# Kernel tuning notes

Hardware: AMD Instinct MI355X
Metric: run time of the kernel (lower is better)

Reference implementation:

```python
import jax, jax.numpy as jnp
import numpy as np

# ---- model hyperparams (from init_kwargs) ----
N_USERS = 200000
N_ITEMS = 100000
DIM = 64
NNZ = 3000000
BATCH = 4096
N_HOPS = 3          # context_hops
EPS = 0.1           # SimGCL perturbation magnitude
TEMP = 0.2          # tau
CL_RATE = 0.5       # lamb
DECAY = 1e-4        # l2


def setup_inputs() -> dict:
    key = jax.random.key(0)
    k = jax.random.split(key, 8)
    user_embed = (jax.random.normal(k[0], (N_USERS, DIM), dtype=jnp.float32) * 0.01)
    item_embed = (jax.random.normal(k[1], (N_ITEMS, DIM), dtype=jnp.float32) * 0.01)
    N = N_USERS + N_ITEMS
    # COO normalized adjacency (buffer, not a parameter in the torch module)
    adj_rows = jax.random.randint(k[2], (NNZ,), 0, N)
    adj_cols = jax.random.randint(k[3], (NNZ,), 0, N)
    adj_vals = jax.random.uniform(k[4], (NNZ,), dtype=jnp.float32) * 0.2
    # unique index batches (torch code calls torch.unique for the CL loss;
    # sampling without replacement makes skipping unique exact, since the
    # InfoNCE mean is permutation invariant)
    users = jax.random.permutation(k[5], N_USERS)[:BATCH].astype(jnp.int32)
    pos_items = jax.random.permutation(k[6], N_ITEMS)[:BATCH].astype(jnp.int32)
    neg_items = jax.random.randint(k[7], (BATCH,), 0, N_ITEMS)
    return {"user_embed": user_embed, "item_embed": item_embed,
            "adj_vals": adj_vals, "adj_rows": adj_rows, "adj_cols": adj_cols,
            "users": users, "pos_items": pos_items, "neg_items": neg_items}


def _spmm(vals, rows, cols, x):
    # torch.sparse.mm(A, x) with A in COO form: out[r] += v * x[c]
    return jax.ops.segment_sum(vals[:, None] * x[cols], rows, num_segments=x.shape[0])


def _gcn(user_embed, item_embed, vals, rows, cols, perturbed, key):
    ego = jnp.concatenate([user_embed, item_embed], axis=0)  # [N, D]
    acc = jnp.zeros_like(ego)
    for h in range(N_HOPS):
        ego = _spmm(vals, rows, cols, ego)
        if perturbed:
            noise = jax.random.uniform(jax.random.fold_in(key, h), ego.shape, dtype=ego.dtype)
            noise = noise / jnp.maximum(jnp.linalg.norm(noise, axis=-1, keepdims=True), 1e-12)
            ego = ego + jnp.sign(ego) * noise * EPS
        acc = acc + ego
    mean = acc / N_HOPS   # stack + mean over hops == running-sum / n_hops
    return mean[:N_USERS], mean[N_USERS:]


def _info_nce(v1, v2, temp):
    v1 = v1 / jnp.maximum(jnp.linalg.norm(v1, axis=1, keepdims=True), 1e-12)
    v2 = v2 / jnp.maximum(jnp.linalg.norm(v2, axis=1, keepdims=True), 1e-12)
    pos = jnp.exp(jnp.sum(v1 * v2, axis=-1) / temp)              # [B]
    ttl = jnp.sum(jnp.exp((v1 @ v2.T) / temp), axis=1)           # [B]
    return jnp.mean(-jnp.log(pos / ttl + 1e-5))


def reference(user_embed, item_embed, adj_vals, adj_rows, adj_cols, users, pos_items, neg_items):
    # --- recommendation branch (no perturbation) ---
    ru, ri = _gcn(user_embed, item_embed, adj_vals, adj_rows, adj_cols, False, jax.random.key(0))
    ue, pe, ne = ru[users], ri[pos_items], ri[neg_items]
    pos_score = jnp.sum(ue * pe, axis=1)
    neg_score = jnp.sum(ue * ne, axis=1)
    rec_loss = jnp.mean(-jnp.log(1e-5 + jax.nn.sigmoid(pos_score - neg_score)))
    reg_loss = DECAY * (jnp.linalg.norm(ue) + jnp.linalg.norm(pe))  # Frobenius norms
    # --- contrastive branch: two perturbed views of the whole GCN ---
    u1, i1 = _gcn(user_embed, item_embed, adj_vals, adj_rows, adj_cols, True, jax.random.key(101))
    u2, i2 = _gcn(user_embed, item_embed, adj_vals, adj_rows, adj_cols, True, jax.random.key(202))
    cl_loss = CL_RATE * (_info_nce(u1[users], u2[users], TEMP)
                         + _info_nce(i1[pos_items], i2[pos_items], TEMP))
    return rec_loss + reg_loss + cl_loss
```

## Files before the change

### kernel.cpp

```cpp
#include <hip/hip_runtime.h>
#include <stdint.h>

#define NUSERS  200000
#define NITEMS  100000
#define NTOT    300000
#define DIM     64
#define NU64    (NUSERS * DIM)
#define NNZC    3000000
#define BATCH   4096
#define B64     (BATCH * DIM)
#define EPSP    0.1f
#define INV_TEMP 5.0f
#define SCAN_ELEMS 1024
#define GELEMS ((size_t)7 * B64 + 2 * BATCH + 8)
#define BCAP   163840

#define BSHIFT 11
#define BROWS  (1 << BSHIFT)
#define NB     ((NTOT + BROWS - 1) / BROWS)
#define CHUNK  4096
#define NCHUNK ((NNZC + CHUNK - 1) / CHUNK)
#define NH     (NB * NCHUNK)
#define CASTB  ((NTOT * DIM) / 2048)
#define Z4V    (NTOT / 4)
#define Z4T    ((2 * BATCH + 8) / 4)
#define ZVB    ((Z4V + 511) / 512)
#define ZTB    ((Z4T + 511) / 512)

typedef short bf16x8 __attribute__((ext_vector_type(8)));
typedef float f32x4  __attribute__((ext_vector_type(4)));

__device__ __forceinline__ float b2f(unsigned short h) {
  return __uint_as_float(((uint32_t)h) << 16);
}
__device__ __forceinline__ unsigned short f2b(float f) {
  uint32_t b = __float_as_uint(f);
  uint32_t r = b + 0x7FFFu + ((b >> 16) & 1u);
  return (unsigned short)(r >> 16);
}

__device__ __forceinline__ uint32_t mix32(uint32_t h) {
  h ^= h >> 16; h *= 0x85EBCA6Bu;
  h ^= h >> 13; h *= 0xC2B2AE35u;
  h ^= h >> 16;
  return h;
}
__device__ __forceinline__ uint32_t noise_key(uint32_t seed, uint32_t hop) {
  return mix32(seed * 0x9E3779B9u + hop * 0x85EBCA6Bu + 0x1BD11BDAu);
}
__device__ __forceinline__ float fast_unif(uint32_t key, uint32_t e) {
  uint32_t h = mix32(key + e * 0x9E3779B9u);
  return __uint_as_float((h >> 9) | 0x3F800000u) - 1.0f;
}
__device__ __forceinline__ float n_ss4(uint32_t key, uint32_t rq, float4& u) {
  uint32_t h = mix32(key + rq * 0x9E3779B9u);
  u.x = ((float)(h & 255u)         + 0.5f) * (1.0f / 256.0f);
  u.y = ((float)((h >> 8) & 255u)  + 0.5f) * (1.0f / 256.0f);
  u.z = ((float)((h >> 16) & 255u) + 0.5f) * (1.0f / 256.0f);
  u.w = ((float)(h >> 24)          + 0.5f) * (1.0f / 256.0f);
  return u.x * u.x + u.y * u.y + u.z * u.z + u.w * u.w;
}

__device__ __forceinline__ float sgnf(float a) {
  return (a > 0.f) ? 1.f : ((a < 0.f) ? -1.f : 0.f);
}

__global__ __launch_bounds__(256) void partA_cast(
    const int* __restrict__ rows, int* __restrict__ Hcnt,
    const float* __restrict__ uemb, const float* __restrict__ iemb,
    unsigned short* __restrict__ X0,
    int* __restrict__ vflag, float* __restrict__ ttlz) {
  int blk = blockIdx.x;
  if (blk >= NCHUNK + CASTB + ZVB) {
    int i4 = (blk - NCHUNK - CASTB - ZVB) * 512 + threadIdx.x;
    float4 z = make_float4(0.f, 0.f, 0.f, 0.f);
    if (i4 < Z4T) ((float4*)ttlz)[i4] = z;
    i4 += 256;
    if (i4 < Z4T) ((float4*)ttlz)[i4] = z;
    return;
  }
  if (blk >= NCHUNK + CASTB) {
    int i4 = (blk - NCHUNK - CASTB) * 512 + threadIdx.x;
    int4 z = make_int4(0, 0, 0, 0);
    if (i4 < Z4V) ((int4*)vflag)[i4] = z;
    i4 += 256;
    if (i4 < Z4V) ((int4*)vflag)[i4] = z;
    return;
  }
  if (blk >= NCHUNK) {
    int base = (blk - NCHUNK) * 2048 + threadIdx.x * 8;
    const float* src = (base < NU64) ? (uemb + base) : (iemb + (base - NU64));
    float4 f0 = ((const float4*)src)[0];
    float4 f1 = ((const float4*)src)[1];
    uint4 o;
    o.x = ((uint32_t)f2b(f0.y) << 16) | f2b(f0.x);
    o.y = ((uint32_t)f2b(f0.w) << 16) | f2b(f0.z);
    o.z = ((uint32_t)f2b(f1.y) << 16) | f2b(f1.x);
    o.w = ((uint32_t)f2b(f1.w) << 16) | f2b(f1.z);
    *(uint4*)(X0 + base) = o;
    return;
  }
  __shared__ int bc[256];
  int c = blk, t = threadIdx.x;
  bc[t] = 0;
  __syncthreads();
  int base = c * CHUNK;
  for (int i = t; i < CHUNK; i += 256) {
    int e = base + i;
    if (e < NNZC) atomicAdd(&bc[rows[e] >> BSHIFT], 1);
  }
  __syncthreads();
  if (t < NB) Hcnt[t * NCHUNK + c] = bc[t];
}

__global__ void scan_block(const int* __restrict__ cnt, int* __restrict__ out,
                           int* __restrict__ bsums, int n) {
  __shared__ int tmp[SCAN_ELEMS];
  int base = blockIdx.x * SCAN_ELEMS;
  int t = threadIdx.x;
  #pragma unroll
  for (int q = 0; q < 4; ++q) {
    int k = t + q * 256, i = base + k;
    tmp[k] = (i < n) ? cnt[i] : 0;
  }
  __syncthreads();
  for (int off = 1; off < SCAN_ELEMS; off <<= 1) {
    int v[4];
    #pragma unroll
    for (int q = 0; q < 4; ++q) {
      int k = t + q * 256;
      v[q] = (k >= off) ? tmp[k - off] : 0;
    }
    __syncthreads();
    #pragma unroll
    for (int q = 0; q < 4; ++q) tmp[t + q * 256] += v[q];
    __syncthreads();
  }
  #pragma unroll
  for (int q = 0; q < 4; ++q) {
    int k = t + q * 256, i = base + k;
    if (i < n) out[i] = (k == 0) ? 0 : tmp[k - 1];
  }
  if (t == 0) bsums[blockIdx.x] = tmp[SCAN_ELEMS - 1];
}

__global__ void add_offsets_scan(int* __restrict__ out,
                                 const int* __restrict__ bsums,
                                 int n, int nb) {
  __shared__ int tmp[512];
  int t = threadIdx.x;
  tmp[t] = (t < nb) ? bsums[t] : 0;
  tmp[t + 256] = (t + 256 < nb) ? bsums[t + 256] : 0;
  __syncthreads();
  for (int off = 1; off < 512; off <<= 1) {
    int v0 = (t >= off) ? tmp[t - off] : 0;
    int v1 = (t + 256 >= off) ? tmp[t + 256 - off] : 0;
    __syncthreads();
    tmp[t] += v0; tmp[t + 256] += v1;
    __syncthreads();
  }
  int i = blockIdx.x * 256 + t;
  if (i < n) {
    int b = i >> 10;
    out[i] += (b == 0) ? 0 : tmp[b - 1];
  }
}

__global__ void add_offsets_emit_scan(int* __restrict__ vmap,
                                      const int* __restrict__ bsums,
                                      const int* __restrict__ vflag,
                                      int* __restrict__ vlist,
                                      int* __restrict__ nV, int nb) {
  __shared__ int tmp[512];
  int t = threadIdx.x;
  tmp[t] = (t < nb) ? bsums[t] : 0;
  tmp[t + 256] = (t + 256 < nb) ? bsums[t + 256] : 0;
  __syncthreads();
  for (int off = 1; off < 512; off <<= 1) {
    int v0 = (t >= off) ? tmp[t - off] : 0;
    int v1 = (t + 256 >= off) ? tmp[t + 256 - off] : 0;
    __syncthreads();
    tmp[t] += v0; tmp[t + 256] += v1;
    __syncthreads();
  }
  int i = blockIdx.x * 256 + t;
  if (i >= NTOT) return;
  int b = i >> 10;
  int m = vmap[i] + ((b == 0) ? 0 : tmp[b - 1]);
  vmap[i] = m;
  if (vflag[i] && m < BCAP) vlist[m] = i;
  if (i == NTOT - 1) {
    int tot = m + vflag[i];
    nV[0] = (tot > BCAP) ? BCAP : tot;
  }
}

__global__ __launch_bounds__(256) void partB(const float* __restrict__ vals,
                                             const int* __restrict__ rows,
                                             const int* __restrict__ cols,
                                             const int* __restrict__ Hofs,
                                             int2* __restrict__ midp,
                                             int* __restrict__ midr) {
  __shared__ int2 stv[CHUNK];
  __shared__ int  str_[CHUNK];
  __shared__ int  cnt[256];
  __shared__ int  sc[256];
  __shared__ int  adj[NB];
  int c = blockIdx.x, t = threadIdx.x;
  cnt[t] = 0;
  __syncthreads();
  int base = c * CHUNK;
  for (int i = t; i < CHUNK; i += 256) {
    int e = base + i;
    if (e < NNZC) atomicAdd(&cnt[rows[e] >> BSHIFT], 1);
  }
  __syncthreads();
  sc[t] = cnt[t];
  __syncthreads();
  for (int off = 1; off < 256; off <<= 1) {
    int u = (t >= off) ? sc[t - off] : 0;
    __syncthreads();
    sc[t] += u;
    __syncthreads();
  }
  int excl = sc[t] - cnt[t];
  cnt[t] = excl;
  if (t < NB) adj[t] = Hofs[t * NCHUNK + c] - excl;
  __syncthreads();
  for (int i = t; i < CHUNK; i += 256) {
    int e = base + i;
    if (e < NNZC) {
      int r = rows[e];
      int b = r >> BSHIFT;
      int p = atomicAdd(&cnt[b], 1);
      stv[p] = make_int2(__float_as_int(vals[e]), cols[e] * DIM);
      str_[p] = r;
    }
  }
  __syncthreads();
  int n = NNZC - base;
  if (n > CHUNK) n = CHUNK;
  for (int p = t; p < n; p += 256) {
    int r = str_[p];
    int b = r >> BSHIFT;
    int dst = adj[b] + p;
    midp[dst] = stv[p];
    midr[dst] = r;
  }
}

__global__ __launch_bounds__(256) void partC(const int2* __restrict__ midp,
                                             const int* __restrict__ midr,
                                             const int* __restrict__ Hofs,
                                             int* __restrict__ rs,
                                             int2* __restrict__ pairs) {
  __shared__ int h[BROWS];
  __shared__ int tsum[256];
  int b = blockIdx.x, t = threadIdx.x;
  int row0 = b << BSHIFT;
  for (int i = t; i < BROWS; i += 256) h[i] = 0;
  __syncthreads();
  int s = Hofs[b * NCHUNK];
  int e = (b + 1 < NB) ? Hofs[(b + 1) * NCHUNK] : NNZC;
  for (int p = s + t; p < e; p += 256)
    atomicAdd(&h[midr[p] - row0], 1);
  __syncthreads();
  int loc[8], run = 0;
  #pragma unroll
  for (int k = 0; k < 8; ++k) { loc[k] = run; run += h[t * 8 + k]; }
  tsum[t] = run;
  __syncthreads();
  for (int off = 1; off < 256; off <<= 1) {
    int v = (t >= off) ? tsum[t - off] : 0;
    __syncthreads();
    tsum[t] += v;
    __syncthreads();
  }
  int baseT = (t == 0) ? 0 : tsum[t - 1];
  #pragma unroll
  for (int k = 0; k < 8; ++k) {
    int i = t * 8 + k;
    int pos = s + baseT + loc[k];
    if (row0 + i < NTOT) rs[row0 + i] = pos;
    h[i] = pos;
  }
  if (b == NB - 1 && t == 0) rs[NTOT] = NNZC;
  __syncthreads();
  for (int p = s + t; p < e; p += 256) {
    int r = midr[p];
    int2 v = midp[p];
    int pos = atomicAdd(&h[r - row0], 1);
    pairs[pos] = v;
  }
}

__global__ __launch_bounds__(256) void mark_v(const int* __restrict__ u,
                                              const int* __restrict__ p,
                                              const int* __restrict__ n,
                                              const int* __restrict__ rs,
                                              const int2* __restrict__ pairs,
                                              int* __restrict__ vflag) {
  int i = blockIdx.x * 256 + threadIdx.x;
  if (i >= 3 * BATCH) return;
  int v = (i < BATCH) ? u[i]
        : (i < 2 * BATCH) ? (NUSERS + p[i - BATCH])
        : (NUSERS + n[i - 2 * BATCH]);
  vflag[v] = 1;
  int s = rs[v], e = rs[v + 1];
  for (int j = s; j < e; ++j) vflag[(unsigned)pairs[j].y >> 6] = 1;
}

__global__ __launch_bounds__(256) void spmm_hop3(
    const int2* __restrict__ pairs, const int* __restrict__ rs,
    const unsigned short* __restrict__ x,
    unsigned short* __restrict__ A, unsigned short* __restrict__ A1,
    unsigned short* __restrict__ A2) {
  const uint32_t k101 = noise_key(101u, 0u);
  const uint32_t k202 = noise_key(202u, 0u);
  int tid  = threadIdx.x;
  int lane = tid & 63;
  int q    = lane & 15;
  int wave = (blockIdx.x * 256 + tid) >> 6;
  int r    = wave * 4 + (lane >> 4);
  int s    = rs[r];
  int e    = rs[r + 1];
  int q4 = q * 4;
  float a0[4] = {0.f, 0.f, 0.f, 0.f};
  for (int j = s; j < e; j += 8) {
    int2 p[8];
    #pragma unroll
    for (int k = 0; k < 8; ++k)
      p[k] = (j + k < e) ? pairs[j + k] : make_int2(0, 0);
    #pragma unroll
    for (int k = 0; k < 8; ++k) {
      float v = __int_as_float(p[k].x);
      unsigned o = (unsigned)(p[k].y + q4);
      ushort4 h = *(const ushort4*)(x + o);
      a0[0] = fmaf(v, b2f(h.x), a0[0]); a0[1] = fmaf(v, b2f(h.y), a0[1]);
      a0[2] = fmaf(v, b2f(h.z), a0[2]); a0[3] = fmaf(v, b2f(h.w), a0[3]);
    }
  }
  int ebase = r * 64 + q4;
  ushort4 st;
  st.x = f2b(a0[0]); st.y = f2b(a0[1]); st.z = f2b(a0[2]); st.w = f2b(a0[3]);
  *(ushort4*)(A + ebase) = st;
  float a[4] = {b2f(st.x), b2f(st.y), b2f(st.z), b2f(st.w)};
  float4 u1, u2;
  float s1 = n_ss4(k101, (uint32_t)(r * 16 + q), u1);
  float s2 = n_ss4(k202, (uint32_t)(r * 16 + q), u2);
  #pragma unroll
  for (int m = 1; m < 16; m <<= 1) {
    s1 += __shfl_xor(s1, m);
    s2 += __shfl_xor(s2, m);
  }
  float sc1 = EPSP / fmaxf(sqrtf(s1), 1e-12f);
  float sc2 = EPSP / fmaxf(sqrtf(s2), 1e-12f);
  float g0 = sgnf(a[0]), g1 = sgnf(a[1]), g2 = sgnf(a[2]), g3 = sgnf(a[3]);
  ushort4 o1, o2;
  o1.x = f2b(fmaf(g0 * u1.x, sc1, a[0]));
  o1.y = f2b(fmaf(g1 * u1.y, sc1, a[1]));
  o1.z = f2b(fmaf(g2 * u1.z, sc1, a[2]));
  o1.w = f2b(fmaf(g3 * u1.w, sc1, a[3]));
  o2.x = f2b(fmaf(g0 * u2.x, sc2, a[0]));
  o2.y = f2b(fmaf(g1 * u2.y, sc2, a[1]));
  o2.z = f2b(fmaf(g2 * u2.z, sc2, a[2]));
  o2.w = f2b(fmaf(g3 * u2.w, sc2, a[3]));
  *(ushort4*)(A1 + ebase) = o1;
  *(ushort4*)(A2 + ebase) = o2;
}

__global__ __launch_bounds__(256) void spmm_sub3t(
    const int2* __restrict__ pairs, const int* __restrict__ rs,
    const int* __restrict__ vlist, const int* __restrict__ nVp,
    const unsigned short* __restrict__ A,
    const unsigned short* __restrict__ A1,
    const unsigned short* __restrict__ A2,
    unsigned short* __restrict__ y0, unsigned short* __restrict__ y1,
    unsigned short* __restrict__ y2) {
  int nV = nVp[0];
  if (blockIdx.x * 16 >= nV) return;
  int tid  = threadIdx.x;
  int lane = tid & 63;
  int q    = lane & 15;
  int wave = (blockIdx.x * 256 + tid) >> 6;
  int slot = wave * 4 + (lane >> 4);
  if (slot >= nV) return;
  int v = vlist[slot];
  int s = rs[v];
  int e = rs[v + 1];
  int q4 = q * 4;
  float c0[4] = {0,0,0,0}, c1[4] = {0,0,0,0}, c2[4] = {0,0,0,0};
  for (int j = s; j < e; j += 8) {
    int2 p[8];
    #pragma unroll
    for (int k = 0; k < 8; ++k)
      p[k] = (j + k < e) ? pairs[j + k] : make_int2(0, 0);
    #pragma unroll
    for (int k = 0; k < 8; ++k) {
      float vv = __int_as_float(p[k].x);
      unsigned o = (unsigned)(p[k].y + q4);
      ushort4 h0 = *(const ushort4*)(A  + o);
      ushort4 h1 = *(const ushort4*)(A1 + o);
      ushort4 h2 = *(const ushort4*)(A2 + o);
      c0[0] = fmaf(vv, b2f(h0.x), c0[0]); c0[1] = fmaf(vv, b2f(h0.y), c0[1]);
      c0[2] = fmaf(vv, b2f(h0.z), c0[2]); c0[3] = fmaf(vv, b2f(h0.w), c0[3]);
      c1[0] = fmaf(vv, b2f(h1.x), c1[0]); c1[1] = fmaf(vv, b2f(h1.y), c1[1]);
      c1[2] = fmaf(vv, b2f(h1.z), c1[2]); c1[3] = fmaf(vv, b2f(h1.w), c1[3]);
      c2[0] = fmaf(vv, b2f(h2.x), c2[0]); c2[1] = fmaf(vv, b2f(h2.y), c2[1]);
      c2[2] = fmaf(vv, b2f(h2.z), c2[2]); c2[3] = fmaf(vv, b2f(h2.w), c2[3]);
    }
  }
  int ob = slot * 64 + q4;
  int en = v * 64 + q4;
  {
    ushort4 st;
    st.x = f2b(c0[0]); st.y = f2b(c0[1]); st.z = f2b(c0[2]); st.w = f2b(c0[3]);
    *(ushort4*)(y0 + ob) = st;
  }
  {
    uint32_t key = noise_key(101u, 1u);
    float u[4], ss = 0.f;
    #pragma unroll
    for (int k = 0; k < 4; ++k) {
      u[k] = fast_unif(key, (uint32_t)(en + k));
      ss += u[k] * u[k];
    }
    #pragma unroll
    for (int msk = 1; msk < 16; msk <<= 1) ss += __shfl_xor(ss, msk);
    float sc = EPSP / fmaxf(sqrtf(ss), 1e-12f);
    #pragma unroll
    for (int k = 0; k < 4; ++k) c1[k] += sgnf(c1[k]) * u[k] * sc;
    ushort4 st;
    st.x = f2b(c1[0]); st.y = f2b(c1[1]); st.z = f2b(c1[2]); st.w = f2b(c1[3]);
    *(ushort4*)(y1 + ob) = st;
  }
  {
    uint32_t key = noise_key(202u, 1u);
    float u[4], ss = 0.f;
    #pragma unroll
    for (int k = 0; k < 4; ++k) {
      u[k] = fast_unif(key, (uint32_t)(en + k));
      ss += u[k] * u[k];
    }
    #pragma unroll
    for (int msk = 1; msk < 16; msk <<= 1) ss += __shfl_xor(ss, msk);
    float sc = EPSP / fmaxf(sqrtf(ss), 1e-12f);
    #pragma unroll
    for (int k = 0; k < 4; ++k) c2[k] += sgnf(c2[k]) * u[k] * sc;
    ushort4 st;
    st.x = f2b(c2[0]); st.y = f2b(c2[1]); st.z = f2b(c2[2]); st.w = f2b(c2[3]);
    *(ushort4*)(y2 + ob) = st;
  }
}

__global__ __launch_bounds__(256) void hop2g3(
    const int2* __restrict__ pairs, const int* __restrict__ rs,
    const unsigned short* __restrict__ Abuf,
    const unsigned short* __restrict__ B0,
    const unsigned short* __restrict__ B1,
    const unsigned short* __restrict__ B2,
    const int* __restrict__ vmap,
    const int* __restrict__ users, const int* __restrict__ pos,
    const int* __restrict__ neg,
    float* __restrict__ g, unsigned short* __restrict__ gb) {
  int seg = blockIdx.y;
  const int* idx = (seg == 0) ? users : ((seg == 1) ? pos : neg);
  int base = (seg == 0) ? 0 : NUSERS;
  int tid  = threadIdx.x;
  int lane = tid & 63;
  int q    = lane & 15;
  int q4 = q * 4;
  int slot = blockIdx.x * 16 + (tid >> 6) * 4 + (lane >> 4);
  int row  = base + idx[slot];
  int s    = rs[row];
  int e    = rs[row + 1];
  bool all3 = (seg < 2);
  float a0[4] = {0,0,0,0}, a1[4] = {0,0,0,0}, a2[4] = {0,0,0,0};
  for (int j = s; j < e; j += 8) {
    int2 p[8];
    #pragma unroll
    for (int k = 0; k < 8; ++k)
      p[k] = (j + k < e) ? pairs[j + k] : make_int2(0, 0);
    int sl[8];
    #pragma unroll
    for (int k = 0; k < 8; ++k)
      sl[k] = vmap[(unsigned)p[k].y >> 6];
    #pragma unroll
    for (int k = 0; k < 8; ++k) {
      float v = __int_as_float(p[k].x);
      unsigned of = (unsigned)(sl[k] * DIM + q4);
      ushort4 h0 = *(const ushort4*)(B0 + of);
      a0[0] = fmaf(v, b2f(h0.x), a0[0]); a0[1] = fmaf(v, b2f(h0.y), a0[1]);
      a0[2] = fmaf(v, b2f(h0.z), a0[2]); a0[3] = fmaf(v, b2f(h0.w), a0[3]);
      if (all3) {
        ushort4 h1 = *(const ushort4*)(B1 + of);
        ushort4 h2 = *(const ushort4*)(B2 + of);
        a1[0] = fmaf(v, b2f(h1.x), a1[0]); a1[1] = fmaf(v, b2f(h1.y), a1[1]);
        a1[2] = fmaf(v, b2f(h1.z), a1[2]); a1[3] = fmaf(v, b2f(h1.w), a1[3]);
        a2[0] = fmaf(v, b2f(h2.x), a2[0]); a2[1] = fmaf(v, b2f(h2.y), a2[1]);
        a2[2] = fmaf(v, b2f(h2.z), a2[2]); a2[3] = fmaf(v, b2f(h2.w), a2[3]);
      }
    }
  }
  size_t rbA = (size_t)row * DIM + q4;
  size_t rbB = (size_t)vmap[row] * DIM + q4;
  ushort4 ha = *(const ushort4*)(Abuf + rbA);
  float af0 = b2f(ha.x), af1 = b2f(ha.y), af2 = b2f(ha.z), af3 = b2f(ha.w);
  {
    ushort4 hb = *(const ushort4*)(B0 + rbB);
    float rv[4];
    rv[0] = (af0 + b2f(hb.x)) + a0[0];
    rv[1] = (af1 + b2f(hb.y)) + a0[1];
    rv[2] = (af2 + b2f(hb.z)) + a0[2];
    rv[3] = (af3 + b2f(hb.w)) + a0[3];
    int og = slot * 64 + q4;
    float* o = g + (size_t)seg * B64;
    *(float4*)(o + og) = make_float4(rv[0], rv[1], rv[2], rv[3]);
  }
  if (!all3) return;
  #pragma unroll
  for (int br = 1; br <= 2; ++br) {
    uint32_t seed = (br == 1) ? 101u : 202u;
    float* ab = (br == 1) ? a1 : a2;
    const unsigned short* Bt = (br == 1) ? B1 : B2;
    {
      uint32_t key = noise_key(seed, 2u);
      int en = row * 64 + q4;
      float u[4], ss = 0.f;
      #pragma unroll
      for (int k = 0; k < 4; ++k) {
        u[k] = fast_unif(key, (uint32_t)(en + k));
        ss += u[k] * u[k];
      }
      #pragma unroll
      for (int msk = 1; msk < 16; msk <<= 1) ss += __shfl_xor(ss, msk);
      float sc = EPSP / fmaxf(sqrtf(ss), 1e-12f);
      #pragma unroll
      for (int k = 0; k < 4; ++k) ab[k] += sgnf(ab[k]) * u[k] * sc;
    }
    float af[4] = {af0, af1, af2, af3};
    {
      uint32_t key0 = noise_key(seed, 0u);
      float4 u;
      float ssn = n_ss4(key0, (uint32_t)(row * 16 + q), u);
      #pragma unroll
      for (int m = 1; m < 16; m <<= 1) ssn += __shfl_xor(ssn, m);
      float scn = EPSP / fmaxf(sqrtf(ssn), 1e-12f);
      af[0] = fmaf(sgnf(af[0]) * u.x, scn, af[0]);
      af[1] = fmaf(sgnf(af[1]) * u.y, scn, af[1]);
      af[2] = fmaf(sgnf(af[2]) * u.z, scn, af[2]);
      af[3] = fmaf(sgnf(af[3]) * u.w, scn, af[3]);
    }
    ushort4 hb = *(const ushort4*)(Bt + rbB);
    float rv[4];
    rv[0] = (af[0] + b2f(hb.x)) + ab[0];
    rv[1] = (af[1] + b2f(hb.y)) + ab[1];
    rv[2] = (af[2] + b2f(hb.z)) + ab[2];
    rv[3] = (af[3] + b2f(hb.w)) + ab[3];
    {
      float ss = rv[0]*rv[0] + rv[1]*rv[1] + rv[2]*rv[2] + rv[3]*rv[3];
      #pragma unroll
      for (int msk = 1; msk < 16; msk <<= 1) ss += __shfl_xor(ss, msk);
      float inv = 1.0f / fmaxf(sqrtf(ss), 1e-12f);
      #pragma unroll
      for (int k = 0; k < 4; ++k) rv[k] *= inv;
    }
    int og = slot * 64 + q4;
    float* o = g + (size_t)(3 + (br - 1) * 2 + seg) * B64;
    *(float4*)(o + og) = make_float4(rv[0], rv[1], rv[2], rv[3]);
    unsigned short* ob = gb + (size_t)((br - 1) * 2 + seg) * B64;
    ushort4 sb;
    sb.x = f2b(rv[0]); sb.y = f2b(rv[1]); sb.z = f2b(rv[2]); sb.w = f2b(rv[3]);
    *(ushort4*)(ob + og) = sb;
  }
}

__global__ __launch_bounds__(256) void nce_ttl_mfma(
    const unsigned short* __restrict__ u1b, const unsigned short* __restrict__ u2b,
    float* __restrict__ tu,
    const unsigned short* __restrict__ w1b, const unsigned short* __restrict__ w2b,
    float* __restrict__ tw) {
  const unsigned short* V1 = (blockIdx.z == 0) ? u1b : w1b;
  const unsigned short* V2 = (blockIdx.z == 0) ? u2b : w2b;
  float* ttl = (blockIdx.z == 0) ? tu : tw;
  int tid  = threadIdx.x;
  int lane = tid & 63;
  int wv   = tid >> 6;
  int lr   = lane & 15;
  int lk   = (lane >> 4) * 8;
  int m0   = blockIdx.x * 64 + wv * 16;
  bf16x8 a0 = *(const bf16x8*)(V1 + (size_t)(m0 + lr) * DIM + lk);
  bf16x8 a1 = *(const bf16x8*)(V1 + (size_t)(m0 + lr) * DIM + 32 + lk);
  float rowsum[4] = {0.f, 0.f, 0.f, 0.f};
  int n0 = blockIdx.y * 256;
  for (int ch = 0; ch < 4; ++ch) {
    int nc = n0 + ch * 64;
    #pragma unroll
    for (int nt = 0; nt < 4; ++nt) {
      int col = nc + nt * 16 + lr;
      bf16x8 b0 = *(const bf16x8*)(V2 + (size_t)col * DIM + lk);
      bf16x8 b1 = *(const bf16x8*)(V2 + (size_t)col * DIM + 32 + lk);
      f32x4 c = {0.f, 0.f, 0.f, 0.f};
      c = __builtin_amdgcn_mfma_f32_16x16x32_bf16(a0, b0, c, 0, 0, 0);
      c = __builtin_amdgcn_mfma_f32_16x16x32_bf16(a1, b1, c, 0, 0, 0);
      #pragma unroll
      for (int rr = 0; rr < 4; ++rr)
        rowsum[rr] += __expf(c[rr] * INV_TEMP);
    }
  }
  #pragma unroll
  for (int rr = 0; rr < 4; ++rr) {
    float s = rowsum[rr];
    #pragma unroll
    for (int m = 1; m < 16; m <<= 1) s += __shfl_xor(s, m);
    rowsum[rr] = s;
  }
  if (lr == 0) {
    int rbase = m0 + (lane >> 4) * 4;
    #pragma unroll
    for (int rr = 0; rr < 4; ++rr)
      atomicAdd(&ttl[rbase + rr], rowsum[rr]);
  }
}

__global__ __launch_bounds__(256) void loss3(const float* __restrict__ g,
                                             const float* __restrict__ ttl_u,
                                             float* __restrict__ acc) {
  __shared__ float red[3][4];
  int role = blockIdx.y;
  int tid = threadIdx.x, lane = tid & 63, wv = tid >> 6;
  int gw = blockIdx.x * 4 + wv;
  if (role == 0) {
    const float* ue = g;
    const float* pe = g + (size_t)B64;
    const float* ne = g + 2 * (size_t)B64;
    const float third = 1.0f / 3.0f;
    float l = 0.f, su = 0.f, sp = 0.f;
    for (int r = gw; r < BATCH; r += 256) {
      int gid = r * 64 + lane;
      float u = ue[gid] * third, p = pe[gid] * third, n = ne[gid] * third;
      float ps = u * p, ns = u * n;
      su += u * u; sp += p * p;
      #pragma unroll
      for (int m = 32; m; m >>= 1) { ps += __shfl_xor(ps, m); ns += __shfl_xor(ns, m); }
      if (lane == 0) {
        float sig = 1.0f / (1.0f + __expf(-(ps - ns)));
        l += -logf(1e-5f + sig);
      }
    }
    #pragma unroll
    for (int m = 32; m; m >>= 1) { su += __shfl_xor(su, m); sp += __shfl_xor(sp, m); }
    if (lane == 0) { red[0][wv] = l; red[1][wv] = su; red[2][wv] = sp; }
    __syncthreads();
    if (tid == 0) {
      atomicAdd(acc + 0, red[0][0] + red[0][1] + red[0][2] + red[0][3]);
      atomicAdd(acc + 1, red[1][0] + red[1][1] + red[1][2] + red[1][3]);
      atomicAdd(acc + 2, red[2][0] + red[2][1] + red[2][2] + red[2][3]);
    }
  } else {
    int by = role - 1;
    const float* v1 = g + (size_t)(3 + by) * B64;
    const float* v2 = g + (size_t)(5 + by) * B64;
    const float* ttl = ttl_u + by * BATCH;
    float l = 0.f;
    for (int r = gw; r < BATCH; r += 256) {
      int gid = r * 64 + lane;
      float p = v1[gid] * v2[gid];
      #pragma unroll
      for (int m = 32; m; m >>= 1) p += __shfl_xor(p, m);
      if (lane == 0) l += -logf(__expf(p * INV_TEMP) / ttl[r] + 1e-5f);
    }
    if (lane == 0) red[0][wv] = l;
    __syncthreads();
    if (tid == 0)
      atomicAdd(acc + 3 + by, red[0][0] + red[0][1] + red[0][2] + red[0][3]);
  }
}

__global__ void finalize_kernel(const float* __restrict__ acc, float* __restrict__ out) {
  out[0] = acc[0] * (1.0f / BATCH)
         + 1e-4f * (sqrtf(acc[1]) + sqrtf(acc[2]))
         + 0.5f * (acc[3] + acc[4]) * (1.0f / BATCH);
}

extern "C" void kernel_launch(void* const* d_in, const int* in_sizes, int n_in,
                              void* d_out, int out_size, void* d_ws, size_t ws_size,
                              hipStream_t stream) {
  (void)in_sizes; (void)n_in; (void)out_size; (void)ws_size;
  const float* user_embed = (const float*)d_in[0];
  const float* item_embed = (const float*)d_in[1];
  const float* adj_vals   = (const float*)d_in[2];
  const int*   adj_rows   = (const int*)d_in[3];
  const int*   adj_cols   = (const int*)d_in[4];
  const int*   users      = (const int*)d_in[5];
  const int*   pos_items  = (const int*)d_in[6];
  const int*   neg_items  = (const int*)d_in[7];
  float* out = (float*)d_out;

  const size_t bufElems = (size_t)NTOT * DIM;
  const size_t bcapE    = (size_t)BCAP * DIM;

  unsigned short* A  = (unsigned short*)d_ws;
  unsigned short* A1 = A + bufElems;
  unsigned short* A2 = A1 + bufElems;
  unsigned short* B0 = A2 + bufElems;
  unsigned short* B1 = B0 + bcapE;
  unsigned short* B2 = B1 + bcapE;
  int2*  pairs = (int2*)(B2 + bcapE);
  float* g     = (float*)(pairs + NNZC);
  int*   rs    = (int*)(g + GELEMS);
  int*   bsums = rs + (NTOT + 4);
  int*   vflag = bsums + 512;
  int*   vmap  = vflag + NTOT;
  int*   vlist = vmap + NTOT;
  int*   nVd   = vlist + NTOT;
  unsigned short* gb =
      (unsigned short*)(((uintptr_t)(nVd + 1) + 31) & ~(uintptr_t)31);

  float* ttl_u = g + 7 * (size_t)B64;
  float* ttl_i = ttl_u + BATCH;
  float* acc   = ttl_u + 2 * BATCH;
  unsigned short* g_u1b = gb + 0 * (size_t)B64;
  unsigned short* g_u2b = gb + 2 * (size_t)B64;
  unsigned short* g_i1b = gb + 1 * (size_t)B64;
  unsigned short* g_i2b = gb + 3 * (size_t)B64;

  int2* midp = (int2*)A;
  int*  midr = (int*)(midp + NNZC);
  int*  Hcnt = midr + NNZC;
  int*  Hofs = Hcnt + NH;
  unsigned short* X0 = B0;

  partA_cast<<<NCHUNK + CASTB + ZVB + ZTB, 256, 0, stream>>>(
      adj_rows, Hcnt, user_embed, item_embed, X0, vflag, ttl_u);
  const int nhb = (NH + SCAN_ELEMS - 1) / SCAN_ELEMS;
  scan_block<<<nhb, 256, 0, stream>>>(Hcnt, Hofs, bsums, NH);
  add_offsets_scan<<<(NH + 255) / 256, 256, 0, stream>>>(Hofs, bsums, NH, nhb);
  partB<<<NCHUNK, 256, 0, stream>>>(adj_vals, adj_rows, adj_cols, Hofs, midp, midr);
  partC<<<NB, 256, 0, stream>>>(midp, midr, Hofs, rs, pairs);

  mark_v<<<(3 * BATCH + 255) / 256, 256, 0, stream>>>(
      users, pos_items, neg_items, rs, pairs, vflag);
  const int nvb = (NTOT + SCAN_ELEMS - 1) / SCAN_ELEMS;
  scan_block<<<nvb, 256, 0, stream>>>(vflag, vmap, bsums, NTOT);
  add_offsets_emit_scan<<<(NTOT + 255) / 256, 256, 0, stream>>>(
      vmap, bsums, vflag, vlist, nVd, nvb);

  const int spmm_blocks = NTOT / 16;

  spmm_hop3<<<spmm_blocks, 256, 0, stream>>>(pairs, rs, X0, A, A1, A2);

  spmm_sub3t<<<spmm_blocks, 256, 0, stream>>>(pairs, rs, vlist, nVd,
                                              A, A1, A2, B0, B1, B2);

  dim3 h2g3(BATCH / 16, 3);
  hop2g3<<<h2g3, 256, 0, stream>>>(pairs, rs, A, B0, B1, B2, vmap,
                                   users, pos_items, neg_items, g, gb);

  dim3 nce_grid(BATCH / 64, BATCH / 256, 2);
  nce_ttl_mfma<<<nce_grid, 256, 0, stream>>>(g_u1b, g_u2b, ttl_u,
                                             g_i1b, g_i2b, ttl_i);
  dim3 lgrid(64, 3);
  loss3<<<lgrid, 256, 0, stream>>>(g, ttl_u, acc);
  finalize_kernel<<<1, 1, 0, stream>>>(acc, out);
}
```

Measured before the change: 485.3 us.

## Build CSR with global per-row atomic histogram and scatter instead of two-pass bucketing

```diff
diff --git a/kernel.cpp b/kernel.cpp
--- a/kernel.cpp
+++ b/kernel.cpp
@@ -15,17 +15,13 @@
 #define GELEMS ((size_t)7 * B64 + 2 * BATCH + 8)
 #define BCAP   163840
 
-#define BSHIFT 11
-#define BROWS  (1 << BSHIFT)
-#define NB     ((NTOT + BROWS - 1) / BROWS)
-#define CHUNK  4096
-#define NCHUNK ((NNZC + CHUNK - 1) / CHUNK)
-#define NH     (NB * NCHUNK)
 #define CASTB  ((NTOT * DIM) / 2048)
 #define Z4V    (NTOT / 4)
 #define Z4T    ((2 * BATCH + 8) / 4)
 #define ZVB    ((Z4V + 511) / 512)
 #define ZTB    ((Z4T + 511) / 512)
+#define HB     2048
+#define HBLKS  ((NNZC + HB - 1) / HB)
 
 typedef short bf16x8 __attribute__((ext_vector_type(8)));
 typedef float f32x4  __attribute__((ext_vector_type(4)));
@@ -65,30 +61,14 @@
   return (a > 0.f) ? 1.f : ((a < 0.f) ? -1.f : 0.f);
 }
 
-__global__ __launch_bounds__(256) void partA_cast(
-    const int* __restrict__ rows, int* __restrict__ Hcnt,
+__global__ __launch_bounds__(256) void cast_zero(
     const float* __restrict__ uemb, const float* __restrict__ iemb,
     unsigned short* __restrict__ X0,
-    int* __restrict__ vflag, float* __restrict__ ttlz) {
+    int* __restrict__ vflag, int* __restrict__ rowcnt,
+    float* __restrict__ ttlz) {
   int blk = blockIdx.x;
-  if (blk >= NCHUNK + CASTB + ZVB) {
-    int i4 = (blk - NCHUNK - CASTB - ZVB) * 512 + threadIdx.x;
-    float4 z = make_float4(0.f, 0.f, 0.f, 0.f);
-    if (i4 < Z4T) ((float4*)ttlz)[i4] = z;
-    i4 += 256;
-    if (i4 < Z4T) ((float4*)ttlz)[i4] = z;
-    return;
-  }
-  if (blk >= NCHUNK + CASTB) {
-    int i4 = (blk - NCHUNK - CASTB) * 512 + threadIdx.x;
-    int4 z = make_int4(0, 0, 0, 0);
-    if (i4 < Z4V) ((int4*)vflag)[i4] = z;
-    i4 += 256;
-    if (i4 < Z4V) ((int4*)vflag)[i4] = z;
-    return;
-  }
-  if (blk >= NCHUNK) {
-    int base = (blk - NCHUNK) * 2048 + threadIdx.x * 8;
+  if (blk < CASTB) {
+    int base = blk * 2048 + threadIdx.x * 8;
     const float* src = (base < NU64) ? (uemb + base) : (iemb + (base - NU64));
     float4 f0 = ((const float4*)src)[0];
     float4 f1 = ((const float4*)src)[1];
@@ -100,17 +80,41 @@
     *(uint4*)(X0 + base) = o;
     return;
   }
-  __shared__ int bc[256];
-  int c = blk, t = threadIdx.x;
-  bc[t] = 0;
-  __syncthreads();
-  int base = c * CHUNK;
-  for (int i = t; i < CHUNK; i += 256) {
+  blk -= CASTB;
+  if (blk < ZVB) {
+    int i4 = blk * 512 + threadIdx.x;
+    int4 z = make_int4(0, 0, 0, 0);
+    if (i4 < Z4V) ((int4*)vflag)[i4] = z;
+    i4 += 256;
+    if (i4 < Z4V) ((int4*)vflag)[i4] = z;
+    return;
+  }
+  blk -= ZVB;
+  if (blk < ZVB) {
+    int i4 = blk * 512 + threadIdx.x;
+    int4 z = make_int4(0, 0, 0, 0);
+    if (i4 < Z4V) ((int4*)rowcnt)[i4] = z;
+    i4 += 256;
+    if (i4 < Z4V) ((int4*)rowcnt)[i4] = z;
+    return;
+  }
+  blk -= ZVB;
+  {
+    int i4 = blk * 512 + threadIdx.x;
+    float4 z = make_float4(0.f, 0.f, 0.f, 0.f);
+    if (i4 < Z4T) ((float4*)ttlz)[i4] = z;
+    i4 += 256;
+    if (i4 < Z4T) ((float4*)ttlz)[i4] = z;
+  }
+}
+
+__global__ __launch_bounds__(256) void row_hist(const int* __restrict__ rows,
+                                                int* __restrict__ rowcnt) {
+  int base = blockIdx.x * HB;
+  for (int i = threadIdx.x; i < HB; i += 256) {
     int e = base + i;
-    if (e < NNZC) atomicAdd(&bc[rows[e] >> BSHIFT], 1);
-  }
-  __syncthreads();
-  if (t < NB) Hcnt[t * NCHUNK + c] = bc[t];
+    if (e < NNZC) atomicAdd(&rowcnt[rows[e]], 1);
+  }
 }
 
 __global__ void scan_block(const int* __restrict__ cnt, int* __restrict__ out,
@@ -144,9 +148,9 @@
   if (t == 0) bsums[blockIdx.x] = tmp[SCAN_ELEMS - 1];
 }
 
-__global__ void add_offsets_scan(int* __restrict__ out,
-                                 const int* __restrict__ bsums,
-                                 int n, int nb) {
+__global__ void add_offsets_rs(int* __restrict__ rs,
+                               const int* __restrict__ bsums,
+                               int* __restrict__ curs, int nb) {
   __shared__ int tmp[512];
   int t = threadIdx.x;
   tmp[t] = (t < nb) ? bsums[t] : 0;
@@ -160,10 +164,12 @@
     __syncthreads();
   }
   int i = blockIdx.x * 256 + t;
-  if (i < n) {
-    int b = i >> 10;
-    out[i] += (b == 0) ? 0 : tmp[b - 1];
-  }
+  if (i >= NTOT) return;
+  int b = i >> 10;
+  int v = rs[i] + ((b == 0) ? 0 : tmp[b - 1]);
+  rs[i] = v;
+  curs[i] = v;
+  if (i == NTOT - 1) rs[NTOT] = NNZC;
 }
 
 __global__ void add_offsets_emit_scan(int* __restrict__ vmap,
@@ -195,102 +201,18 @@
   }
 }
 
-__global__ __launch_bounds__(256) void partB(const float* __restrict__ vals,
-                                             const int* __restrict__ rows,
-                                             const int* __restrict__ cols,
-                                             const int* __restrict__ Hofs,
-                                             int2* __restrict__ midp,
-                                             int* __restrict__ midr) {
-  __shared__ int2 stv[CHUNK];
-  __shared__ int  str_[CHUNK];
-  __shared__ int  cnt[256];
-  __shared__ int  sc[256];
-  __shared__ int  adj[NB];
-  int c = blockIdx.x, t = threadIdx.x;
-  cnt[t] = 0;
-  __syncthreads();
-  int base = c * CHUNK;
-  for (int i = t; i < CHUNK; i += 256) {
-    int e = base + i;
-    if (e < NNZC) atomicAdd(&cnt[rows[e] >> BSHIFT], 1);
-  }
-  __syncthreads();
-  sc[t] = cnt[t];
-  __syncthreads();
-  for (int off = 1; off < 256; off <<= 1) {
-    int u = (t >= off) ? sc[t - off] : 0;
-    __syncthreads();
-    sc[t] += u;
-    __syncthreads();
-  }
-  int excl = sc[t] - cnt[t];
-  cnt[t] = excl;
-  if (t < NB) adj[t] = Hofs[t * NCHUNK + c] - excl;
-  __syncthreads();
-  for (int i = t; i < CHUNK; i += 256) {
+__global__ __launch_bounds__(256) void place_pairs(
+    const float* __restrict__ vals, const int* __restrict__ rows,
+    const int* __restrict__ cols, int* __restrict__ curs,
+    int2* __restrict__ pairs) {
+  int base = blockIdx.x * HB;
+  for (int i = threadIdx.x; i < HB; i += 256) {
     int e = base + i;
     if (e < NNZC) {
       int r = rows[e];
-      int b = r >> BSHIFT;
-      int p = atomicAdd(&cnt[b], 1);
-      stv[p] = make_int2(__float_as_int(vals[e]), cols[e] * DIM);
-      str_[p] = r;
-    }
-  }
-  __syncthreads();
-  int n = NNZC - base;
-  if (n > CHUNK) n = CHUNK;
-  for (int p = t; p < n; p += 256) {
-    int r = str_[p];
-    int b = r >> BSHIFT;
-    int dst = adj[b] + p;
-    midp[dst] = stv[p];
-    midr[dst] = r;
-  }
-}
-
-__global__ __launch_bounds__(256) void partC(const int2* __restrict__ midp,
-                                             const int* __restrict__ midr,
-                                             const int* __restrict__ Hofs,
-                                             int* __restrict__ rs,
-                                             int2* __restrict__ pairs) {
-  __shared__ int h[BROWS];
-  __shared__ int tsum[256];
-  int b = blockIdx.x, t = threadIdx.x;
-  int row0 = b << BSHIFT;
-  for (int i = t; i < BROWS; i += 256) h[i] = 0;
-  __syncthreads();
-  int s = Hofs[b * NCHUNK];
-  int e = (b + 1 < NB) ? Hofs[(b + 1) * NCHUNK] : NNZC;
-  for (int p = s + t; p < e; p += 256)
-    atomicAdd(&h[midr[p] - row0], 1);
-  __syncthreads();
-  int loc[8], run = 0;
-  #pragma unroll
-  for (int k = 0; k < 8; ++k) { loc[k] = run; run += h[t * 8 + k]; }
-  tsum[t] = run;
-  __syncthreads();
-  for (int off = 1; off < 256; off <<= 1) {
-    int v = (t >= off) ? tsum[t - off] : 0;
-    __syncthreads();
-    tsum[t] += v;
-    __syncthreads();
-  }
-  int baseT = (t == 0) ? 0 : tsum[t - 1];
-  #pragma unroll
-  for (int k = 0; k < 8; ++k) {
-    int i = t * 8 + k;
-    int pos = s + baseT + loc[k];
-    if (row0 + i < NTOT) rs[row0 + i] = pos;
-    h[i] = pos;
-  }
-  if (b == NB - 1 && t == 0) rs[NTOT] = NNZC;
-  __syncthreads();
-  for (int p = s + t; p < e; p += 256) {
-    int r = midr[p];
-    int2 v = midp[p];
-    int pos = atomicAdd(&h[r - row0], 1);
-    pairs[pos] = v;
+      int pos = atomicAdd(&curs[r], 1);
+      pairs[pos] = make_int2(__float_as_int(vals[e]), cols[e] * DIM);
+    }
   }
 }
 
@@ -714,34 +636,32 @@
   int*   vmap  = vflag + NTOT;
   int*   vlist = vmap + NTOT;
   int*   nVd   = vlist + NTOT;
+  int*   rowcnt = nVd + 4;
+  int*   curs   = rowcnt + NTOT;
   unsigned short* gb =
-      (unsigned short*)(((uintptr_t)(nVd + 1) + 31) & ~(uintptr_t)31);
+      (unsigned short*)(((uintptr_t)(curs + NTOT) + 31) & ~(uintptr_t)31);
 
   float* ttl_u = g + 7 * (size_t)B64;
   float* ttl_i = ttl_u + BATCH;
   float* acc   = ttl_u + 2 * BATCH;
   unsigned short* g_u1b = gb + 0 * (size_t)B64;
+  unsigned short* g_i1b = gb + 1 * (size_t)B64;
   unsigned short* g_u2b = gb + 2 * (size_t)B64;
-  unsigned short* g_i1b = gb + 1 * (size_t)B64;
   unsigned short* g_i2b = gb + 3 * (size_t)B64;
 
-  int2* midp = (int2*)A;
-  int*  midr = (int*)(midp + NNZC);
-  int*  Hcnt = midr + NNZC;
-  int*  Hofs = Hcnt + NH;
   unsigned short* X0 = B0;
 
-  partA_cast<<<NCHUNK + CASTB + ZVB + ZTB, 256, 0, stream>>>(
-      adj_rows, Hcnt, user_embed, item_embed, X0, vflag, ttl_u);
-  const int nhb = (NH + SCAN_ELEMS - 1) / SCAN_ELEMS;
-  scan_block<<<nhb, 256, 0, stream>>>(Hcnt, Hofs, bsums, NH);
-  add_offsets_scan<<<(NH + 255) / 256, 256, 0, stream>>>(Hofs, bsums, NH, nhb);
-  partB<<<NCHUNK, 256, 0, stream>>>(adj_vals, adj_rows, adj_cols, Hofs, midp, midr);
-  partC<<<NB, 256, 0, stream>>>(midp, midr, Hofs, rs, pairs);
+  cast_zero<<<CASTB + 2 * ZVB + ZTB, 256, 0, stream>>>(
+      user_embed, item_embed, X0, vflag, rowcnt, ttl_u);
+  row_hist<<<HBLKS, 256, 0, stream>>>(adj_rows, rowcnt);
+  const int nvb = (NTOT + SCAN_ELEMS - 1) / SCAN_ELEMS;
+  scan_block<<<nvb, 256, 0, stream>>>(rowcnt, rs, bsums, NTOT);
+  add_offsets_rs<<<(NTOT + 255) / 256, 256, 0, stream>>>(rs, bsums, curs, nvb);
+  place_pairs<<<HBLKS, 256, 0, stream>>>(adj_vals, adj_rows, adj_cols,
+                                         curs, pairs);
 
   mark_v<<<(3 * BATCH + 255) / 256, 256, 0, stream>>>(
       users, pos_items, neg_items, rs, pairs, vflag);
-  const int nvb = (NTOT + SCAN_ELEMS - 1) / SCAN_ELEMS;
   scan_block<<<nvb, 256, 0, stream>>>(vflag, vmap, bsums, NTOT);
   add_offsets_emit_scan<<<(NTOT + 255) / 256, 256, 0, stream>>>(
       vmap, bsums, vflag, vlist, nVd, nvb);
```

Result: slower. 660.6 us (+36.1%).

## Pack local row index into column field and use finer row buckets

Applied to the files above, without the earlier changes.

```diff
diff --git a/kernel.cpp b/kernel.cpp
--- a/kernel.cpp
+++ b/kernel.cpp
@@ -15,7 +15,7 @@
 #define GELEMS ((size_t)7 * B64 + 2 * BATCH + 8)
 #define BCAP   163840
 
-#define BSHIFT 11
+#define BSHIFT 9
 #define BROWS  (1 << BSHIFT)
 #define NB     ((NTOT + BROWS - 1) / BROWS)
 #define CHUNK  4096
@@ -100,9 +100,10 @@
     *(uint4*)(X0 + base) = o;
     return;
   }
-  __shared__ int bc[256];
+  __shared__ int bc[1024];
   int c = blk, t = threadIdx.x;
-  bc[t] = 0;
+  #pragma unroll
+  for (int q = 0; q < 4; ++q) bc[t + q * 256] = 0;
   __syncthreads();
   int base = c * CHUNK;
   for (int i = t; i < CHUNK; i += 256) {
@@ -110,7 +111,7 @@
     if (e < NNZC) atomicAdd(&bc[rows[e] >> BSHIFT], 1);
   }
   __syncthreads();
-  if (t < NB) Hcnt[t * NCHUNK + c] = bc[t];
+  for (int i = t; i < NB; i += 256) Hcnt[i * NCHUNK + c] = bc[i];
 }
 
 __global__ void scan_block(const int* __restrict__ cnt, int* __restrict__ out,
@@ -199,15 +200,15 @@
                                              const int* __restrict__ rows,
                                              const int* __restrict__ cols,
                                              const int* __restrict__ Hofs,
-                                             int2* __restrict__ midp,
-                                             int* __restrict__ midr) {
-  __shared__ int2 stv[CHUNK];
-  __shared__ int  str_[CHUNK];
-  __shared__ int  cnt[256];
-  __shared__ int  sc[256];
-  __shared__ int  adj[NB];
+                                             int2* __restrict__ midp) {
+  __shared__ int2  stv[CHUNK];
+  __shared__ short stb[CHUNK];
+  __shared__ int   cnt[1024];
+  __shared__ int   sc[1024];
+  __shared__ int   adj[1024];
   int c = blockIdx.x, t = threadIdx.x;
-  cnt[t] = 0;
+  #pragma unroll
+  for (int q = 0; q < 4; ++q) cnt[t + q * 256] = 0;
   __syncthreads();
   int base = c * CHUNK;
   for (int i = t; i < CHUNK; i += 256) {
@@ -215,17 +216,28 @@
     if (e < NNZC) atomicAdd(&cnt[rows[e] >> BSHIFT], 1);
   }
   __syncthreads();
-  sc[t] = cnt[t];
-  __syncthreads();
-  for (int off = 1; off < 256; off <<= 1) {
-    int u = (t >= off) ? sc[t - off] : 0;
-    __syncthreads();
-    sc[t] += u;
-    __syncthreads();
-  }
-  int excl = sc[t] - cnt[t];
-  cnt[t] = excl;
-  if (t < NB) adj[t] = Hofs[t * NCHUNK + c] - excl;
+  #pragma unroll
+  for (int q = 0; q < 4; ++q) sc[t + q * 256] = cnt[t + q * 256];
+  __syncthreads();
+  for (int off = 1; off < 1024; off <<= 1) {
+    int v[4];
+    #pragma unroll
+    for (int q = 0; q < 4; ++q) {
+      int k = t + q * 256;
+      v[q] = (k >= off) ? sc[k - off] : 0;
+    }
+    __syncthreads();
+    #pragma unroll
+    for (int q = 0; q < 4; ++q) sc[t + q * 256] += v[q];
+    __syncthreads();
+  }
+  #pragma unroll
+  for (int q = 0; q < 4; ++q) {
+    int k = t + q * 256;
+    int excl = sc[k] - cnt[k];
+    if (k < NB) adj[k] = Hofs[k * NCHUNK + c] - excl;
+    cnt[k] = excl;
+  }
   __syncthreads();
   for (int i = t; i < CHUNK; i += 256) {
     int e = base + i;
@@ -233,24 +245,21 @@
       int r = rows[e];
       int b = r >> BSHIFT;
       int p = atomicAdd(&cnt[b], 1);
-      stv[p] = make_int2(__float_as_int(vals[e]), cols[e] * DIM);
-      str_[p] = r;
+      stv[p] = make_int2(__float_as_int(vals[e]),
+                         ((r & (BROWS - 1)) << 19) | cols[e]);
+      stb[p] = (short)b;
     }
   }
   __syncthreads();
   int n = NNZC - base;
   if (n > CHUNK) n = CHUNK;
   for (int p = t; p < n; p += 256) {
-    int r = str_[p];
-    int b = r >> BSHIFT;
-    int dst = adj[b] + p;
-    midp[dst] = stv[p];
-    midr[dst] = r;
+    int b = stb[p];
+    midp[adj[b] + p] = stv[p];
   }
 }
 
 __global__ __launch_bounds__(256) void partC(const int2* __restrict__ midp,
-                                             const int* __restrict__ midr,
                                              const int* __restrict__ Hofs,
                                              int* __restrict__ rs,
                                              int2* __restrict__ pairs) {
@@ -258,17 +267,15 @@
   __shared__ int tsum[256];
   int b = blockIdx.x, t = threadIdx.x;
   int row0 = b << BSHIFT;
-  for (int i = t; i < BROWS; i += 256) h[i] = 0;
+  h[t] = 0; h[t + 256] = 0;
   __syncthreads();
   int s = Hofs[b * NCHUNK];
   int e = (b + 1 < NB) ? Hofs[(b + 1) * NCHUNK] : NNZC;
   for (int p = s + t; p < e; p += 256)
-    atomicAdd(&h[midr[p] - row0], 1);
-  __syncthreads();
-  int loc[8], run = 0;
-  #pragma unroll
-  for (int k = 0; k < 8; ++k) { loc[k] = run; run += h[t * 8 + k]; }
-  tsum[t] = run;
+    atomicAdd(&h[(unsigned)midp[p].y >> 19], 1);
+  __syncthreads();
+  int l0 = h[t * 2], l1 = h[t * 2 + 1];
+  tsum[t] = l0 + l1;
   __syncthreads();
   for (int off = 1; off < 256; off <<= 1) {
     int v = (t >= off) ? tsum[t - off] : 0;
@@ -276,21 +283,19 @@
     tsum[t] += v;
     __syncthreads();
   }
-  int baseT = (t == 0) ? 0 : tsum[t - 1];
-  #pragma unroll
-  for (int k = 0; k < 8; ++k) {
-    int i = t * 8 + k;
-    int pos = s + baseT + loc[k];
-    if (row0 + i < NTOT) rs[row0 + i] = pos;
-    h[i] = pos;
-  }
+  int baseT = s + ((t == 0) ? 0 : tsum[t - 1]);
+  int i0 = t * 2, i1 = t * 2 + 1;
+  int pos0 = baseT, pos1 = baseT + l0;
+  if (row0 + i0 < NTOT) rs[row0 + i0] = pos0;
+  if (row0 + i1 < NTOT) rs[row0 + i1] = pos1;
+  h[i0] = pos0; h[i1] = pos1;
   if (b == NB - 1 && t == 0) rs[NTOT] = NNZC;
   __syncthreads();
   for (int p = s + t; p < e; p += 256) {
-    int r = midr[p];
     int2 v = midp[p];
-    int pos = atomicAdd(&h[r - row0], 1);
-    pairs[pos] = v;
+    int rl = (unsigned)v.y >> 19;
+    int pos = atomicAdd(&h[rl], 1);
+    pairs[pos] = make_int2(v.x, (v.y & 0x7FFFF) << 6);
   }
 }
 
@@ -715,19 +720,18 @@
   int*   vlist = vmap + NTOT;
   int*   nVd   = vlist + NTOT;
   unsigned short* gb =
-      (unsigned short*)(((uintptr_t)(nVd + 1) + 31) & ~(uintptr_t)31);
+      (unsigned short*)(((uintptr_t)(nVd + 4) + 31) & ~(uintptr_t)31);
 
   float* ttl_u = g + 7 * (size_t)B64;
   float* ttl_i = ttl_u + BATCH;
   float* acc   = ttl_u + 2 * BATCH;
   unsigned short* g_u1b = gb + 0 * (size_t)B64;
+  unsigned short* g_i1b = gb + 1 * (size_t)B64;
   unsigned short* g_u2b = gb + 2 * (size_t)B64;
-  unsigned short* g_i1b = gb + 1 * (size_t)B64;
   unsigned short* g_i2b = gb + 3 * (size_t)B64;
 
   int2* midp = (int2*)A;
-  int*  midr = (int*)(midp + NNZC);
-  int*  Hcnt = midr + NNZC;
+  int*  Hcnt = (int*)(midp + NNZC);
   int*  Hofs = Hcnt + NH;
   unsigned short* X0 = B0;
 
@@ -736,8 +740,8 @@
   const int nhb = (NH + SCAN_ELEMS - 1) / SCAN_ELEMS;
   scan_block<<<nhb, 256, 0, stream>>>(Hcnt, Hofs, bsums, NH);
   add_offsets_scan<<<(NH + 255) / 256, 256, 0, stream>>>(Hofs, bsums, NH, nhb);
-  partB<<<NCHUNK, 256, 0, stream>>>(adj_vals, adj_rows, adj_cols, Hofs, midp, midr);
-  partC<<<NB, 256, 0, stream>>>(midp, midr, Hofs, rs, pairs);
+  partB<<<NCHUNK, 256, 0, stream>>>(adj_vals, adj_rows, adj_cols, Hofs, midp);
+  partC<<<NB, 256, 0, stream>>>(midp, Hofs, rs, pairs);
 
   mark_v<<<(3 * BATCH + 255) / 256, 256, 0, stream>>>(
       users, pos_items, neg_items, rs, pairs, vflag);
```

New measurement: 464.0 us. 4.4% less time.
